# Optimization experiments

Hardware: AMD Instinct MI355X
Metric: run time of the kernel (lower is better)

## Reference

```python
import jax, jax.numpy as jnp
import numpy as np

B, S, D, H, FF = 2, 2048, 1024, 16, 4096
HD = D // H          # head dim = 64
ROT = HD // 2        # rotary dim = dim/(num_heads*2) = 32 (partial rotation)
EPS = 1e-5


def setup_inputs() -> dict:
    key = jax.random.key(0)
    ks = jax.random.split(key, 16)
    std = 0.02
    return {
        "x": jax.random.normal(ks[0], (B, S, D), jnp.float32),
        "mask": jnp.ones((B, 1, 1, S), jnp.int32),
        "wq": jax.random.normal(ks[1], (D, D), jnp.float32) * std,
        "bq": jnp.zeros((D,), jnp.float32),
        "wk": jax.random.normal(ks[2], (D, D), jnp.float32) * std,
        "bk": jnp.zeros((D,), jnp.float32),
        "wv": jax.random.normal(ks[3], (D, D), jnp.float32) * std,
        "bv": jnp.zeros((D,), jnp.float32),
        "wo": jax.random.normal(ks[4], (D, D), jnp.float32) * std,
        "bo": jnp.zeros((D,), jnp.float32),
        "ln1_w": jnp.ones((D,), jnp.float32),
        "ln1_b": jnp.zeros((D,), jnp.float32),
        "ln2_w": jnp.ones((D,), jnp.float32),
        "ln2_b": jnp.zeros((D,), jnp.float32),
        "w1": jax.random.normal(ks[5], (D, FF), jnp.float32) * std,
        "b1": jnp.zeros((FF,), jnp.float32),
        "w2": jax.random.normal(ks[6], (FF, D), jnp.float32) * std,
        "b2": jnp.zeros((D,), jnp.float32),
    }


def _layernorm(x, w, b):
    mu = jnp.mean(x, axis=-1, keepdims=True)
    var = jnp.mean(jnp.square(x - mu), axis=-1, keepdims=True)
    return (x - mu) * jax.lax.rsqrt(var + EPS) * w + b


def _rope(t):
    # t: [B, H, S, HD]; rotate first ROT features, interleaved (GPT-J) pairing
    inv_freq = 1.0 / (10000.0 ** (jnp.arange(0, ROT, 2, dtype=jnp.float32) / ROT))
    ang = jnp.arange(S, dtype=jnp.float32)[:, None] * inv_freq      # [S, ROT//2]
    ang = jnp.repeat(ang, 2, axis=-1)                               # [S, ROT]
    cos, sin = jnp.cos(ang), jnp.sin(ang)
    t_rot, t_pass = t[..., :ROT], t[..., ROT:]
    pr = t_rot.reshape(*t_rot.shape[:-1], ROT // 2, 2)
    rot = jnp.stack([-pr[..., 1], pr[..., 0]], axis=-1).reshape(t_rot.shape)
    return jnp.concatenate([t_rot * cos + rot * sin, t_pass], axis=-1)


def reference(x, mask, wq, bq, wk, bk, wv, bv, wo, bo,
              ln1_w, ln1_b, ln2_w, ln2_b, w1, b1, w2, b2):
    res = x
    h = _layernorm(x, ln1_w, ln1_b)
    q = (h @ wq + bq).reshape(B, S, H, HD).transpose(0, 2, 1, 3)
    k = (h @ wk + bk).reshape(B, S, H, HD).transpose(0, 2, 1, 3)
    v = (h @ wv + bv).reshape(B, S, H, HD).transpose(0, 2, 1, 3)
    q, k = _rope(q), _rope(k)
    score = jnp.einsum('bhqd,bhkd->bhqk', q, k) * (1.0 / np.sqrt(HD))
    score = jnp.where(mask == 0, jnp.float32(-1e9), score)
    attn = jax.nn.softmax(score, axis=-1)
    out = jnp.einsum('bhqk,bhkd->bhqd', attn, v)
    out = out.transpose(0, 2, 1, 3).reshape(B, S, D) @ wo + bo
    x = res + out
    res = x
    h = _layernorm(x, ln2_w, ln2_b)
    h = jax.nn.gelu(h @ w1 + b1, approximate=False) @ w2 + b2
    return res + h
```

## Files before the change

kernel.cpp:

```cpp
#include <hip/hip_runtime.h>
#include <cstdint>
#include <cstddef>


typedef __bf16 bf16;
typedef __bf16 bf16x2 __attribute__((ext_vector_type(2)));
typedef __bf16 bf16x4v __attribute__((ext_vector_type(4)));
typedef __bf16 bf16x8 __attribute__((ext_vector_type(8)));
typedef float  f32x4  __attribute__((ext_vector_type(4)));

#define NB 2
#define NS 2048
#define ND 1024
#define NH 16
#define NHD 64
#define NFF 4096
#define NM (NB*NS)
#define QKSCALE 0.18033688011112042f

typedef uint32_t __attribute__((address_space(1))) gu32_t;
typedef uint32_t __attribute__((address_space(3))) lu32_t;
__device__ __forceinline__ void async_copy16(void* lds, const void* g) {
  __builtin_amdgcn_global_load_lds((gu32_t*)g, (lu32_t*)lds, 16, 0, 0);
}

__device__ __forceinline__ float gelu_f(float x) {
  return 0.5f * x * (1.0f + erff(x * 0.70710678118654752f));
}

__global__ __launch_bounds__(256) void prep_kernel(
    const float* __restrict__ wq, const float* __restrict__ wk,
    const float* __restrict__ wv, const float* __restrict__ wo,
    const float* __restrict__ w1, const float* __restrict__ w2,
    bf16* __restrict__ wqt, bf16* __restrict__ wkt, bf16* __restrict__ wvt,
    bf16* __restrict__ wot, bf16* __restrict__ w1t, bf16* __restrict__ w2t,
    const float* __restrict__ bq, const float* __restrict__ bk,
    const float* __restrict__ bv, float* __restrict__ bcat,
    const int* __restrict__ mask, float* __restrict__ m01f,
    bf16* __restrict__ m01b, float2* __restrict__ rtab,
    const float* __restrict__ x, const float* __restrict__ ln1w,
    const float* __restrict__ ln1b, bf16* __restrict__ h1) {
  int flat = blockIdx.x;
  int t = threadIdx.x;
  if (flat < 12288) {
    __shared__ float tile[32][33];
    const float* W; bf16* Wt; long bx, by; int K, N;
    if (flat < 4096) {
      int which = flat >> 10, r = flat & 1023;
      const float* Ws[4] = {wq, wk, wv, wo};
      bf16* Wts[4] = {wqt, wkt, wvt, wot};
      W = Ws[which]; Wt = Wts[which]; bx = r & 31; by = r >> 5; K = ND; N = ND;
    } else if (flat < 8192) {
      int r = flat - 4096;
      W = w1; Wt = w1t; bx = r & 127; by = r >> 7; K = ND; N = NFF;
    } else {
      int r = flat - 8192;
      W = w2; Wt = w2t; bx = r & 31; by = r >> 5; K = NFF; N = ND;
    }
    int tx = t & 31, ty = t >> 5;
#pragma unroll
    for (int r = 0; r < 4; ++r)
      tile[ty + r*8][tx] = W[(by*32 + ty + r*8) * (long)N + bx*32 + tx];
    __syncthreads();
#pragma unroll
    for (int r = 0; r < 4; ++r)
      Wt[(bx*32 + ty + r*8) * (long)K + by*32 + tx] = (bf16)tile[tx][ty + r*8];
  } else if (flat < 12444) {
    int blk = flat - 12288;
    if (blk < 12) {
      int i = blk * 256 + t;
      bcat[i] = (i < ND) ? bq[i] : ((i < 2*ND) ? bk[i - ND] : bv[i - 2*ND]);
    } else if (blk < 28) {
      int i = (blk - 12) * 256 + t;
      float v = mask[i] ? 1.0f : 0.0f;
      m01f[i] = v;
      m01b[i] = (bf16)v;
    } else {
      int idx = (blk - 28) * 256 + t;
      int s = idx >> 4, i = idx & 15;
      float ang = (float)s * exp2f(-(float)i * (13.287712379549449f / 16.0f));
      float sn, cs;
      sincosf(ang, &sn, &cs);
      rtab[idx] = make_float2(cs, sn);
    }
  } else {
    long row = flat - 12444;
    float4 v = ((const float4*)(x + row*ND))[t];
    float s  = v.x + v.y + v.z + v.w;
    float sq = v.x*v.x + v.y*v.y + v.z*v.z + v.w*v.w;
#pragma unroll
    for (int m = 1; m <= 32; m <<= 1) { s += __shfl_xor(s, m); sq += __shfl_xor(sq, m); }
    __shared__ float ss[4], ssq[4];
    if ((t & 63) == 0) { ss[t>>6] = s; ssq[t>>6] = sq; }
    __syncthreads();
    s  = ss[0] + ss[1] + ss[2] + ss[3];
    sq = ssq[0] + ssq[1] + ssq[2] + ssq[3];
    float mu = s * (1.0f/ND);
    float rs = rsqrtf(sq * (1.0f/ND) - mu*mu + 1e-5f);
    float4 wv4 = ((const float4*)ln1w)[t];
    float4 bv4 = ((const float4*)ln1b)[t];
    bf16x4v o;
    o[0] = (bf16)((v.x-mu)*rs*wv4.x + bv4.x);
    o[1] = (bf16)((v.y-mu)*rs*wv4.y + bv4.y);
    o[2] = (bf16)((v.z-mu)*rs*wv4.z + bv4.z);
    o[3] = (bf16)((v.w-mu)*rs*wv4.w + bv4.w);
    *(bf16x4v*)(h1 + row*ND + t*4) = o;
  }
}

__global__ __launch_bounds__(256) void vtrans_kernel(
    const bf16* __restrict__ v, bf16* __restrict__ vt) {
  __shared__ bf16 t[64][66];
  int st = blockIdx.x, bh = blockIdx.y;
  int b = bh >> 4, h = bh & 15;
  int c = threadIdx.x & 63, rg = threadIdx.x >> 6;
  const bf16* src = v + ((long)b*NS + st*64)*ND + h*64;
#pragma unroll
  for (int i = 0; i < 16; ++i) {
    int r = rg*16 + i;
    t[r][c] = src[(long)r*ND + c];
  }
  __syncthreads();
  bf16* dst = vt + (long)bh*64*NS + st*64;
#pragma unroll
  for (int i = 0; i < 16; ++i) {
    int d = rg*16 + i;
    dst[(long)d*NS + c] = t[c][d];
  }
}

__global__ __launch_bounds__(256) void ln_kernel(
    const float* __restrict__ x, const float* __restrict__ w,
    const float* __restrict__ b, bf16* __restrict__ out) {
  long row = blockIdx.x;
  int t = threadIdx.x;
  float4 v = ((const float4*)(x + row*ND))[t];
  float s  = v.x + v.y + v.z + v.w;
  float sq = v.x*v.x + v.y*v.y + v.z*v.z + v.w*v.w;
#pragma unroll
  for (int m = 1; m <= 32; m <<= 1) { s += __shfl_xor(s, m); sq += __shfl_xor(sq, m); }
  __shared__ float ss[4], ssq[4];
  if ((t & 63) == 0) { ss[t>>6] = s; ssq[t>>6] = sq; }
  __syncthreads();
  s  = ss[0] + ss[1] + ss[2] + ss[3];
  sq = ssq[0] + ssq[1] + ssq[2] + ssq[3];
  float mu = s * (1.0f/ND);
  float rs = rsqrtf(sq * (1.0f/ND) - mu*mu + 1e-5f);
  float4 wv = ((const float4*)w)[t];
  float4 bv = ((const float4*)b)[t];
  bf16x4v o;
  o[0] = (bf16)((v.x-mu)*rs*wv.x + bv.x);
  o[1] = (bf16)((v.y-mu)*rs*wv.y + bv.y);
  o[2] = (bf16)((v.z-mu)*rs*wv.z + bv.z);
  o[3] = (bf16)((v.w-mu)*rs*wv.w + bv.w);
  *(bf16x4v*)(out + row*ND + t*4) = o;
}

__global__ __launch_bounds__(256) void ffn2red_kernel(
    const float* __restrict__ P, const float* __restrict__ y1,
    const float* __restrict__ b2, float* __restrict__ out) {
  const long n4 = (long)NM * ND / 4;
  const float4* p = (const float4*)P;
  const float4* y = (const float4*)y1;
  const float4* bb = (const float4*)b2;
  float4* o = (float4*)out;
  for (long i = (long)blockIdx.x*256 + threadIdx.x; i < n4;
       i += (long)gridDim.x*256) {
    float4 a0 = p[i], a1 = p[i + n4], a2 = p[i + 2*n4], a3 = p[i + 3*n4];
    float4 yv = y[i];
    float4 bv = bb[i & 255];
    float4 r;
    r.x = (a0.x + a1.x) + (a2.x + a3.x) + yv.x + bv.x;
    r.y = (a0.y + a1.y) + (a2.y + a3.y) + yv.y + bv.y;
    r.z = (a0.z + a1.z) + (a2.z + a3.z) + yv.z + bv.z;
    r.w = (a0.w + a1.w) + (a2.w + a3.w) + yv.w + bv.w;
    o[i] = r;
  }
}

template<int EPI>
__global__ __launch_bounds__(512, 2) void gemm256_kernel(
    const bf16* __restrict__ A, const bf16* __restrict__ Bt,
    const float* __restrict__ bias, void* __restrict__ Cout,
    const float2* __restrict__ rtab, const float* __restrict__ m01f,
    int M, int N, int K, int lda, int ldbt) {
  __shared__ __align__(16) bf16 Alds[2][256*32];
  __shared__ __align__(16) bf16 Blds[2][256*32];
  const int tid = threadIdx.x, lane = tid & 63, w = tid >> 6;
  const int fr = lane & 15, kg = lane >> 4;
  const int wr = w >> 2, wc = w & 3;
  const int swb = (kg ^ ((fr >> 1) & 3)) << 4;
  const int kz = (EPI == 2) ? blockIdx.z : 0;
  const long kofs = (long)kz * K;

  const int gx = gridDim.x;
  int lin = blockIdx.y * gx + blockIdx.x;
  int nwg = gx * gridDim.y;
  int swz = (lin & 7) * (nwg >> 3) + (lin >> 3);
  const long am0 = (long)(swz / gx) * 256;
  const long bn0 = (long)(swz % gx) * 256;

  const f32x4 fzero = {0.f, 0.f, 0.f, 0.f};
  f32x4 acc[8][4];
#pragma unroll
  for (int m = 0; m < 8; ++m)
#pragma unroll
    for (int n = 0; n < 4; ++n) acc[m][n] = fzero;

  auto stage = [&](int kt, int bufi) {
#pragma unroll
    for (int i = 0; i < 2; ++i) {
      int s = i*512 + tid;
      int r = s >> 2, c = (s & 3) ^ ((s >> 3) & 3);
      async_copy16((char*)&Alds[bufi][0] + i*8192 + w*1024,
                   &A[(am0 + r)*(long)lda + kofs + kt + c*8]);
      async_copy16((char*)&Blds[bufi][0] + i*8192 + w*1024,
                   &Bt[(bn0 + r)*(long)ldbt + kofs + kt + c*8]);
    }
  };

  const int nk = K >> 5;
  stage(0, 0);
  asm volatile("s_waitcnt vmcnt(0)" ::: "memory");
  __builtin_amdgcn_s_barrier();
  __builtin_amdgcn_sched_barrier(0);

  for (int t = 0; t < nk; ++t) {
    const int cur = t & 1;
    if (t + 1 < nk) stage((t + 1) * 32, cur ^ 1);
    const char* Ab = (const char*)&Alds[cur][0];
    const char* Bb = (const char*)&Blds[cur][0];
    bf16x8 af[4], bfv[4];
#pragma unroll
    for (int n = 0; n < 4; ++n) bfv[n] = *(const bf16x8*)(Bb + (wc*64 + n*16 + fr)*64 + swb);
#pragma unroll
    for (int m = 0; m < 4; ++m) af[m]  = *(const bf16x8*)(Ab + (wr*128 + m*16 + fr)*64 + swb);
    asm volatile("s_waitcnt lgkmcnt(0)" ::: "memory");
    __builtin_amdgcn_sched_barrier(0);
    __builtin_amdgcn_s_setprio(1);
#pragma unroll
    for (int m = 0; m < 4; ++m)
#pragma unroll
      for (int n = 0; n < 4; ++n)
        acc[m][n] = __builtin_amdgcn_mfma_f32_16x16x32_bf16(af[m], bfv[n], acc[m][n], 0, 0, 0);
    __builtin_amdgcn_s_setprio(0);
#pragma unroll
    for (int m = 0; m < 4; ++m) af[m] = *(const bf16x8*)(Ab + (wr*128 + (m+4)*16 + fr)*64 + swb);
    asm volatile("s_waitcnt lgkmcnt(0)" ::: "memory");
    __builtin_amdgcn_sched_barrier(0);
    __builtin_amdgcn_s_setprio(1);
#pragma unroll
    for (int m = 0; m < 4; ++m)
#pragma unroll
      for (int n = 0; n < 4; ++n)
        acc[m+4][n] = __builtin_amdgcn_mfma_f32_16x16x32_bf16(af[m], bfv[n], acc[m+4][n], 0, 0, 0);
    __builtin_amdgcn_s_setprio(0);
    asm volatile("s_waitcnt vmcnt(0)" ::: "memory");
    __builtin_amdgcn_s_barrier();
    __builtin_amdgcn_sched_barrier(0);
  }

  const int rbase = kg * 4;
  const int region = (int)(bn0 >> 10);
#pragma unroll
  for (int m = 0; m < 8; ++m) {
#pragma unroll
    for (int n = 0; n < 4; ++n) {
      long col = bn0 + wc*64 + n*16 + fr;
      float bia = (EPI == 2) ? 0.0f : bias[col];
#pragma unroll
      for (int j = 0; j < 4; ++j) {
        long row = am0 + wr*128 + m*16 + rbase + j;
        float val = acc[m][n][j] + bia;
        if (EPI == 1) {
          ((bf16*)Cout)[row * N + col] = (bf16)gelu_f(val);
        } else if (EPI == 2) {
          ((float*)Cout)[((long)kz * NM + row) * N + col] = val;
        } else {
          long cv = col & 1023;
          if (region <= 1) {
            float pval = __shfl_xor(val, 1);
            if (n < 2) {
              float2 cs = rtab[((row & (NS-1)) << 4) | ((n*16 + fr) >> 1)];
              val = (fr & 1) ? val*cs.x + pval*cs.y : val*cs.x - pval*cs.y;
            }
            if (region == 0) val *= QKSCALE;
          } else {
            val *= m01f[row];
          }
          ((bf16*)Cout)[(long)region * (NM*(long)ND) + row * ND + cv] = (bf16)val;
        }
      }
    }
  }
}

__global__ __launch_bounds__(512, 1) void gemm128x8_kernel(
    const bf16* __restrict__ A, const bf16* __restrict__ Bt,
    const float* __restrict__ bias, const float* __restrict__ res,
    float* __restrict__ Cout, int M, int N, int K) {
  __shared__ __align__(16) bf16 Alds[4][128*64];
  __shared__ __align__(16) bf16 Blds[4][128*64];
  const int tid = threadIdx.x, lane = tid & 63, w = tid >> 6;
  const int fr = lane & 15, kg = lane >> 4;
  const int wr = w >> 1, wc = w & 1;

  const int gx = gridDim.x;
  int lin = blockIdx.y * gx + blockIdx.x;
  int nwg = gx * gridDim.y;
  int swz = (lin & 7) * (nwg >> 3) + (lin >> 3);
  const long am0 = (long)(swz / gx) * 128;
  const long bn0 = (long)(swz % gx) * 128;

  const f32x4 fzero = {0.f, 0.f, 0.f, 0.f};
  f32x4 acc[2][4];
#pragma unroll
  for (int m = 0; m < 2; ++m)
#pragma unroll
    for (int n = 0; n < 4; ++n) acc[m][n] = fzero;

  auto stage = [&](int kt, int bufi) {
#pragma unroll
    for (int i = 0; i < 2; ++i) {
      int s = i*512 + tid;
      int r = s >> 3, c = (s & 7) ^ (r & 7);
      async_copy16((char*)&Alds[bufi][0] + i*8192 + w*1024,
                   &A[(am0 + r)*K + kt + c*8]);
      async_copy16((char*)&Blds[bufi][0] + i*8192 + w*1024,
                   &Bt[(bn0 + r)*K + kt + c*8]);
    }
  };

  const int nk = K >> 6;
  stage(0, 0);
  stage(64, 1);
  asm volatile("s_waitcnt vmcnt(4)" ::: "memory");
  __builtin_amdgcn_s_barrier();
  __builtin_amdgcn_sched_barrier(0);

  for (int t = 0; t < nk; ++t) {
    const int cur = t & 3;
    if (t + 2 < nk) stage((t + 2) * 64, (t + 2) & 3);
    const char* Ab = (const char*)&Alds[cur][0];
    const char* Bb = (const char*)&Blds[cur][0];
    bf16x8 af[2][2], bfv[2][4];
#pragma unroll
    for (int kk = 0; kk < 2; ++kk) {
#pragma unroll
      for (int m = 0; m < 2; ++m) {
        int r = wr*32 + m*16 + fr;
        af[kk][m] = *(const bf16x8*)(Ab + r*128 + (((kk*4 + kg) ^ (r & 7)) << 4));
      }
#pragma unroll
      for (int n = 0; n < 4; ++n) {
        int r = wc*64 + n*16 + fr;
        bfv[kk][n] = *(const bf16x8*)(Bb + r*128 + (((kk*4 + kg) ^ (r & 7)) << 4));
      }
    }
    asm volatile("s_waitcnt lgkmcnt(0)" ::: "memory");
    __builtin_amdgcn_sched_barrier(0);
    __builtin_amdgcn_s_setprio(1);
#pragma unroll
    for (int kk = 0; kk < 2; ++kk)
#pragma unroll
      for (int m = 0; m < 2; ++m)
#pragma unroll
        for (int n = 0; n < 4; ++n)
          acc[m][n] = __builtin_amdgcn_mfma_f32_16x16x32_bf16(af[kk][m], bfv[kk][n], acc[m][n], 0, 0, 0);
    __builtin_amdgcn_s_setprio(0);
    if (t + 2 < nk) { asm volatile("s_waitcnt vmcnt(4)" ::: "memory"); }
    else            { asm volatile("s_waitcnt vmcnt(0)" ::: "memory"); }
    __builtin_amdgcn_s_barrier();
    __builtin_amdgcn_sched_barrier(0);
  }

  const int rbase = kg * 4;
#pragma unroll
  for (int m = 0; m < 2; ++m) {
#pragma unroll
    for (int n = 0; n < 4; ++n) {
      long col = bn0 + wc*64 + n*16 + fr;
      float bia = bias[col];
#pragma unroll
      for (int j = 0; j < 4; ++j) {
        long row = am0 + wr*32 + m*16 + rbase + j;
        Cout[row * N + col] = acc[m][n][j] + bia + res[row * N + col];
      }
    }
  }
}

__global__ __launch_bounds__(512) void attn_kernel(
    const bf16* __restrict__ q, const bf16* __restrict__ k,
    const bf16* __restrict__ vt, const bf16* __restrict__ m01b,
    bf16* __restrict__ out) {
  int lin = blockIdx.y * 16 + blockIdx.x;
  int swz = (lin & 7) * 64 + (lin >> 3);
  const int qt = swz & 15;
  const int bh = swz >> 4;
  const int b = bh >> 4, h = bh & 15;
  const int tid = threadIdx.x, lane = tid & 63, w = tid >> 6;
  const int fr = lane & 15, kg = lane >> 4;
  const int k8 = kg * 8;
  const int frl = fr & 3, frh = fr >> 2;

  __shared__ __align__(16) bf16 Klds[3][64*64];
  __shared__ __align__(16) bf16 Vlds[3][64*64];
  __shared__ __align__(16) bf16 Mlds[NS];

  const long qrow = (long)qt*128 + w*16 + fr;
  const bf16* qbase = q + ((long)b*NS + qrow)*ND + h*NHD;
  bf16x8 qf[2];
  qf[0] = *(const bf16x8*)(qbase + k8);
  qf[1] = *(const bf16x8*)(qbase + 32 + k8);

  const bf16* kbase = k + (long)b*NS*ND + h*NHD;
  const bf16* vtb = vt + (long)bh*64*NS;
  const bf16* mbase = m01b + (long)b*NS;

  if (w < 4) async_copy16((char*)Mlds + w*1024, mbase + tid*8);

  const int srow = tid >> 3, sc = tid & 7;
  const int csK = (sc ^ (srow & 7) ^ (((srow >> 3) & 1) << 2));
  const int csV = (sc ^ (srow & 7));
  auto stageK = [&](int kt, int bufi) {
    async_copy16((char*)&Klds[bufi][0] + w*1024,
                 kbase + ((long)kt*64 + srow)*ND + csK*8);
  };
  auto stageV = [&](int kt, int bufi) {
    async_copy16((char*)&Vlds[bufi][0] + w*1024,
                 vtb + (long)srow*NS + kt*64 + csV*8);
  };

  const f32x4 fzero = {0.f, 0.f, 0.f, 0.f};
  f32x4 oacc[4], oaccL = fzero;
#pragma unroll
  for (int n = 0; n < 4; ++n) oacc[n] = fzero;

  stageK(0, 0); stageV(0, 0);
  stageK(1, 1); stageV(1, 1);
  asm volatile("s_waitcnt vmcnt(2)" ::: "memory");
  __builtin_amdgcn_s_barrier();
  __builtin_amdgcn_sched_barrier(0);

  const int NT = NS / 64;
  int bcur = 0, bpre = 1;
  for (int kt = 0; kt < NT; ++kt) {
    if (kt + 2 < NT) {
      bpre = (bpre == 2) ? 0 : bpre + 1;
      stageK(kt + 2, bpre);
      stageV(kt + 2, bpre);
    }
    const char* Kb = (const char*)&Klds[bcur][0];
    const char* Vb = (const char*)&Vlds[bcur][0];

    bf16x8 vbm0 = *(const bf16x8*)&Mlds[kt*64 + k8];
    bf16x8 vbm1 = *(const bf16x8*)&Mlds[kt*64 + 32 + k8];

    f32x4 sacc[4];
#pragma unroll
    for (int n = 0; n < 4; ++n) sacc[n] = fzero;
#pragma unroll
    for (int n = 0; n < 4; ++n) {
      int r = (frh << 3) + ((n & 1) << 2) + frl + ((n >> 1) << 5);
      int swzr = (r & 7) ^ (((r >> 3) & 1) << 2);
#pragma unroll
      for (int kk = 0; kk < 2; ++kk) {
        bf16x8 kf = *(const bf16x8*)(Kb + r*128 + ((((kk << 2) | kg) ^ swzr) << 4));
        sacc[n] = __builtin_amdgcn_mfma_f32_16x16x32_bf16(kf, qf[kk], sacc[n], 0, 0, 0);
      }
    }

    float p[4][4];
#pragma unroll
    for (int n = 0; n < 4; ++n) {
      p[n][0] = exp2f(sacc[n][0]);
      p[n][1] = exp2f(sacc[n][1]);
      p[n][2] = exp2f(sacc[n][2]);
      p[n][3] = exp2f(sacc[n][3]);
    }

    bf16x8 paf[2];
#pragma unroll
    for (int n = 0; n < 4; ++n) {
#pragma unroll
      for (int j = 0; j < 4; ++j)
        paf[n >> 1][((n & 1) << 2) + j] = (bf16)p[n][j];
    }

    oaccL = __builtin_amdgcn_mfma_f32_16x16x32_bf16(paf[0], vbm0, oaccL, 0, 0, 0);
    oaccL = __builtin_amdgcn_mfma_f32_16x16x32_bf16(paf[1], vbm1, oaccL, 0, 0, 0);

#pragma unroll
    for (int kk = 0; kk < 2; ++kk) {
#pragma unroll
      for (int n2 = 0; n2 < 4; ++n2) {
        int r = n2*16 + fr;
        bf16x8 vb8 = *(const bf16x8*)(Vb + r*128 + ((((kk << 2) | kg) ^ (r & 7)) << 4));
        oacc[n2] = __builtin_amdgcn_mfma_f32_16x16x32_bf16(paf[kk], vb8, oacc[n2], 0, 0, 0);
      }
    }

    if (kt + 2 < NT)      { asm volatile("s_waitcnt vmcnt(2)" ::: "memory"); }
    else if (kt + 1 < NT) { asm volatile("s_waitcnt vmcnt(0)" ::: "memory"); }
    __builtin_amdgcn_s_barrier();
    __builtin_amdgcn_sched_barrier(0);
    bcur = (bcur == 2) ? 0 : bcur + 1;
  }

#pragma unroll
  for (int j = 0; j < 4; ++j) {
    float inv = 1.0f / oaccL[j];
    long orow = (long)qt*128 + w*16 + kg*4 + j;
    bf16* ob = out + ((long)b*NS + orow)*ND + h*NHD;
#pragma unroll
    for (int n2 = 0; n2 < 4; ++n2) ob[n2*16 + fr] = (bf16)(oacc[n2][j] * inv);
  }
}

extern "C" void kernel_launch(void* const* d_in, const int* in_sizes, int n_in,
                              void* d_out, int out_size, void* d_ws, size_t ws_size,
                              hipStream_t stream) {
  const float* x    = (const float*)d_in[0];
  const int*   mask = (const int*)d_in[1];
  const float* wq   = (const float*)d_in[2];
  const float* bq   = (const float*)d_in[3];
  const float* wk   = (const float*)d_in[4];
  const float* bk   = (const float*)d_in[5];
  const float* wv   = (const float*)d_in[6];
  const float* bv   = (const float*)d_in[7];
  const float* wo   = (const float*)d_in[8];
  const float* bo   = (const float*)d_in[9];
  const float* ln1w = (const float*)d_in[10];
  const float* ln1b = (const float*)d_in[11];
  const float* ln2w = (const float*)d_in[12];
  const float* ln2b = (const float*)d_in[13];
  const float* w1   = (const float*)d_in[14];
  const float* b1   = (const float*)d_in[15];
  const float* w2   = (const float*)d_in[16];
  const float* b2   = (const float*)d_in[17];
  float* out = (float*)d_out;

  char* ws = (char*)d_ws;
  const size_t MB = 1024ull * 1024ull;
  bf16* wqt = (bf16*)(ws + 0*MB);
  bf16* wkt = (bf16*)(ws + 2*MB);
  bf16* wvt = (bf16*)(ws + 4*MB);
  bf16* wot = (bf16*)(ws + 6*MB);
  bf16* w1t = (bf16*)(ws + 8*MB);
  bf16* w2t = (bf16*)(ws + 16*MB);
  bf16* h1   = (bf16*)(ws + 24*MB);
  bf16* qb   = (bf16*)(ws + 32*MB);
  bf16* kb   = (bf16*)(ws + 40*MB);
  bf16* vb   = (bf16*)(ws + 48*MB);
  bf16* vtb  = h1;
  bf16* attnb = (bf16*)(ws + 72*MB);
  bf16* f1   = (bf16*)(ws + 24*MB);
  float* y1  = (float*)(ws + 56*MB);
  bf16* h2   = (bf16*)(ws + 72*MB);
  float* bcat = (float*)(ws + 80*MB);
  float* m01f = (float*)(ws + 80*MB + 16*1024);
  bf16*  m01b = (bf16*) (ws + 80*MB + 32*1024);
  float2* rtab = (float2*)(ws + 80*MB + 48*1024);
  float* pK   = (float*)(ws + 84*MB);
  const bool use_splitk = (ws_size >= 148ull*MB);
  (void)in_sizes; (void)n_in; (void)out_size;

  prep_kernel<<<16540, 256, 0, stream>>>(wq, wk, wv, wo, w1, w2,
                                         wqt, wkt, wvt, wot, w1t, w2t,
                                         bq, bk, bv, bcat, mask, m01f, m01b,
                                         rtab, x, ln1w, ln1b, h1);

  gemm256_kernel<3><<<dim3(12, 16), 512, 0, stream>>>(h1, wqt, bcat, qb,
                                                      rtab, m01f, NM, 3*ND, ND,
                                                      ND, ND);
  vtrans_kernel<<<dim3(32, 32), 256, 0, stream>>>(vb, vtb);

  attn_kernel<<<dim3(16, 32), 512, 0, stream>>>(qb, kb, vtb, m01b, attnb);

  gemm128x8_kernel<<<dim3(8, 32), 512, 0, stream>>>(attnb, wot, bo, x, y1,
                                                    NM, ND, ND);
  ln_kernel<<<NM, 256, 0, stream>>>(y1, ln2w, ln2b, h2);
  gemm256_kernel<1><<<dim3(16, 16), 512, 0, stream>>>(h2, w1t, b1, f1,
                                                      nullptr, nullptr,
                                                      NM, NFF, ND, ND, ND);
  if (use_splitk) {
    gemm256_kernel<2><<<dim3(4, 16, 4), 512, 0, stream>>>(f1, w2t, nullptr, pK,
                                                          nullptr, nullptr,
                                                          NM, ND, ND, NFF, NFF);
    ffn2red_kernel<<<2048, 256, 0, stream>>>(pK, y1, b2, out);
  } else {
    gemm128x8_kernel<<<dim3(8, 32), 512, 0, stream>>>(f1, w2t, b2, y1, out,
                                                      NM, ND, NFF);
  }
}
```

Measured before the change: 292.0 us.

## Deepen GEMM K-tile to 64 and prefetch two stages ahead

```diff
diff --git a/kernel.cpp b/kernel.cpp
--- a/kernel.cpp
+++ b/kernel.cpp
@@ -184,12 +184,11 @@
     const float* __restrict__ bias, void* __restrict__ Cout,
     const float2* __restrict__ rtab, const float* __restrict__ m01f,
     int M, int N, int K, int lda, int ldbt) {
-  __shared__ __align__(16) bf16 Alds[2][256*32];
-  __shared__ __align__(16) bf16 Blds[2][256*32];
+  __shared__ __align__(16) bf16 Alds[2][256*64];
+  __shared__ __align__(16) bf16 Blds[2][256*64];
   const int tid = threadIdx.x, lane = tid & 63, w = tid >> 6;
   const int fr = lane & 15, kg = lane >> 4;
   const int wr = w >> 2, wc = w & 3;
-  const int swb = (kg ^ ((fr >> 1) & 3)) << 4;
   const int kz = (EPI == 2) ? blockIdx.z : 0;
   const long kofs = (long)kz * K;
 
@@ -209,32 +208,42 @@
 
   auto stage = [&](int kt, int bufi) {
 #pragma unroll
-    for (int i = 0; i < 2; ++i) {
+    for (int i = 0; i < 4; ++i) {
       int s = i*512 + tid;
-      int r = s >> 2, c = (s & 3) ^ ((s >> 3) & 3);
+      int r = s >> 3, c = (s & 7) ^ (r & 7);
       async_copy16((char*)&Alds[bufi][0] + i*8192 + w*1024,
                    &A[(am0 + r)*(long)lda + kofs + kt + c*8]);
+    }
+#pragma unroll
+    for (int i = 0; i < 4; ++i) {
+      int s = i*512 + tid;
+      int r = s >> 3, c = (s & 7) ^ (r & 7);
       async_copy16((char*)&Blds[bufi][0] + i*8192 + w*1024,
                    &Bt[(bn0 + r)*(long)ldbt + kofs + kt + c*8]);
     }
   };
 
-  const int nk = K >> 5;
+  const int nk = K >> 6;
   stage(0, 0);
-  asm volatile("s_waitcnt vmcnt(0)" ::: "memory");
+  stage(64, 1);
+  asm volatile("s_waitcnt vmcnt(8)" ::: "memory");
   __builtin_amdgcn_s_barrier();
   __builtin_amdgcn_sched_barrier(0);
 
   for (int t = 0; t < nk; ++t) {
-    const int cur = t & 1;
-    if (t + 1 < nk) stage((t + 1) * 32, cur ^ 1);
-    const char* Ab = (const char*)&Alds[cur][0];
-    const char* Bb = (const char*)&Blds[cur][0];
-    bf16x8 af[4], bfv[4];
-#pragma unroll
-    for (int n = 0; n < 4; ++n) bfv[n] = *(const bf16x8*)(Bb + (wc*64 + n*16 + fr)*64 + swb);
-#pragma unroll
-    for (int m = 0; m < 4; ++m) af[m]  = *(const bf16x8*)(Ab + (wr*128 + m*16 + fr)*64 + swb);
+    const char* Ab = (const char*)&Alds[t & 1][0];
+    const char* Bb = (const char*)&Blds[t & 1][0];
+    bf16x8 bfv0[4], bfv1[4], af[4];
+#pragma unroll
+    for (int n = 0; n < 4; ++n) {
+      int r = wc*64 + n*16 + fr;
+      bfv0[n] = *(const bf16x8*)(Bb + r*128 + ((kg ^ (r & 7)) << 4));
+    }
+#pragma unroll
+    for (int m = 0; m < 4; ++m) {
+      int r = wr*128 + m*16 + fr;
+      af[m] = *(const bf16x8*)(Ab + r*128 + ((kg ^ (r & 7)) << 4));
+    }
     asm volatile("s_waitcnt lgkmcnt(0)" ::: "memory");
     __builtin_amdgcn_sched_barrier(0);
     __builtin_amdgcn_s_setprio(1);
@@ -242,10 +251,18 @@
     for (int m = 0; m < 4; ++m)
 #pragma unroll
       for (int n = 0; n < 4; ++n)
-        acc[m][n] = __builtin_amdgcn_mfma_f32_16x16x32_bf16(af[m], bfv[n], acc[m][n], 0, 0, 0);
+        acc[m][n] = __builtin_amdgcn_mfma_f32_16x16x32_bf16(af[m], bfv0[n], acc[m][n], 0, 0, 0);
     __builtin_amdgcn_s_setprio(0);
 #pragma unroll
-    for (int m = 0; m < 4; ++m) af[m] = *(const bf16x8*)(Ab + (wr*128 + (m+4)*16 + fr)*64 + swb);
+    for (int n = 0; n < 4; ++n) {
+      int r = wc*64 + n*16 + fr;
+      bfv1[n] = *(const bf16x8*)(Bb + r*128 + (((4 + kg) ^ (r & 7)) << 4));
+    }
+#pragma unroll
+    for (int m = 0; m < 4; ++m) {
+      int r = wr*128 + m*16 + fr;
+      af[m] = *(const bf16x8*)(Ab + r*128 + (((4 + kg) ^ (r & 7)) << 4));
+    }
     asm volatile("s_waitcnt lgkmcnt(0)" ::: "memory");
     __builtin_amdgcn_sched_barrier(0);
     __builtin_amdgcn_s_setprio(1);
@@ -253,9 +270,46 @@
     for (int m = 0; m < 4; ++m)
 #pragma unroll
       for (int n = 0; n < 4; ++n)
-        acc[m+4][n] = __builtin_amdgcn_mfma_f32_16x16x32_bf16(af[m], bfv[n], acc[m+4][n], 0, 0, 0);
+        acc[m][n] = __builtin_amdgcn_mfma_f32_16x16x32_bf16(af[m], bfv1[n], acc[m][n], 0, 0, 0);
     __builtin_amdgcn_s_setprio(0);
-    asm volatile("s_waitcnt vmcnt(0)" ::: "memory");
+#pragma unroll
+    for (int m = 0; m < 4; ++m) {
+      int r = wr*128 + (m+4)*16 + fr;
+      af[m] = *(const bf16x8*)(Ab + r*128 + ((kg ^ (r & 7)) << 4));
+    }
+    asm volatile("s_waitcnt lgkmcnt(0)" ::: "memory");
+    __builtin_amdgcn_sched_barrier(0);
+    __builtin_amdgcn_s_setprio(1);
+#pragma unroll
+    for (int m = 0; m < 4; ++m)
+#pragma unroll
+      for (int n = 0; n < 4; ++n)
+        acc[m+4][n] = __builtin_amdgcn_mfma_f32_16x16x32_bf16(af[m], bfv0[n], acc[m+4][n], 0, 0, 0);
+    __builtin_amdgcn_s_setprio(0);
+#pragma unroll
+    for (int m = 0; m < 4; ++m) {
+      int r = wr*128 + (m+4)*16 + fr;
+      af[m] = *(const bf16x8*)(Ab + r*128 + (((4 + kg) ^ (r & 7)) << 4));
+    }
+    asm volatile("s_waitcnt lgkmcnt(0)" ::: "memory");
+    __builtin_amdgcn_sched_barrier(0);
+    __builtin_amdgcn_s_setprio(1);
+#pragma unroll
+    for (int m = 0; m < 4; ++m)
+#pragma unroll
+      for (int n = 0; n < 4; ++n)
+        acc[m+4][n] = __builtin_amdgcn_mfma_f32_16x16x32_bf16(af[m], bfv1[n], acc[m+4][n], 0, 0, 0);
+    __builtin_amdgcn_s_setprio(0);
+
+    if (t + 1 == nk) break;
+    __builtin_amdgcn_s_barrier();
+    __builtin_amdgcn_sched_barrier(0);
+    if (t + 2 < nk) {
+      stage((t + 2) * 64, t & 1);
+      asm volatile("s_waitcnt vmcnt(8)" ::: "memory");
+    } else {
+      asm volatile("s_waitcnt vmcnt(0)" ::: "memory");
+    }
     __builtin_amdgcn_s_barrier();
     __builtin_amdgcn_sched_barrier(0);
   }
```

Result: faster. 274.2 us (-6.1%).

## Deepen GEMM LDS pipeline to four buffers and store split-K partials in bf16

Applied to the files above, without the earlier changes.

```diff
diff --git a/kernel.cpp b/kernel.cpp
--- a/kernel.cpp
+++ b/kernel.cpp
@@ -157,24 +157,31 @@
 }
 
 __global__ __launch_bounds__(256) void ffn2red_kernel(
-    const float* __restrict__ P, const float* __restrict__ y1,
+    const bf16* __restrict__ P, const float* __restrict__ y1,
     const float* __restrict__ b2, float* __restrict__ out) {
-  const long n4 = (long)NM * ND / 4;
-  const float4* p = (const float4*)P;
-  const float4* y = (const float4*)y1;
-  const float4* bb = (const float4*)b2;
-  float4* o = (float4*)out;
-  for (long i = (long)blockIdx.x*256 + threadIdx.x; i < n4;
+  const long n8 = (long)NM * ND / 8;
+  for (long i = (long)blockIdx.x*256 + threadIdx.x; i < n8;
        i += (long)gridDim.x*256) {
-    float4 a0 = p[i], a1 = p[i + n4], a2 = p[i + 2*n4], a3 = p[i + 3*n4];
-    float4 yv = y[i];
-    float4 bv = bb[i & 255];
-    float4 r;
-    r.x = (a0.x + a1.x) + (a2.x + a3.x) + yv.x + bv.x;
-    r.y = (a0.y + a1.y) + (a2.y + a3.y) + yv.y + bv.y;
-    r.z = (a0.z + a1.z) + (a2.z + a3.z) + yv.z + bv.z;
-    r.w = (a0.w + a1.w) + (a2.w + a3.w) + yv.w + bv.w;
-    o[i] = r;
+    bf16x8 p0 = ((const bf16x8*)P)[i];
+    bf16x8 p1 = ((const bf16x8*)P)[i + n8];
+    bf16x8 p2 = ((const bf16x8*)P)[i + 2*n8];
+    bf16x8 p3 = ((const bf16x8*)P)[i + 3*n8];
+    float4 ya = ((const float4*)y1)[2*i];
+    float4 yb = ((const float4*)y1)[2*i + 1];
+    int cb = (int)((i * 8) & 1023);
+    float4 ba = *(const float4*)&b2[cb];
+    float4 bb = *(const float4*)&b2[cb + 4];
+    float4 ra, rb;
+    ra.x = ((float)p0[0]+(float)p1[0])+((float)p2[0]+(float)p3[0]) + ya.x + ba.x;
+    ra.y = ((float)p0[1]+(float)p1[1])+((float)p2[1]+(float)p3[1]) + ya.y + ba.y;
+    ra.z = ((float)p0[2]+(float)p1[2])+((float)p2[2]+(float)p3[2]) + ya.z + ba.z;
+    ra.w = ((float)p0[3]+(float)p1[3])+((float)p2[3]+(float)p3[3]) + ya.w + ba.w;
+    rb.x = ((float)p0[4]+(float)p1[4])+((float)p2[4]+(float)p3[4]) + yb.x + bb.x;
+    rb.y = ((float)p0[5]+(float)p1[5])+((float)p2[5]+(float)p3[5]) + yb.y + bb.y;
+    rb.z = ((float)p0[6]+(float)p1[6])+((float)p2[6]+(float)p3[6]) + yb.z + bb.z;
+    rb.w = ((float)p0[7]+(float)p1[7])+((float)p2[7]+(float)p3[7]) + yb.w + bb.w;
+    ((float4*)out)[2*i]     = ra;
+    ((float4*)out)[2*i + 1] = rb;
   }
 }
 
@@ -184,12 +191,11 @@
     const float* __restrict__ bias, void* __restrict__ Cout,
     const float2* __restrict__ rtab, const float* __restrict__ m01f,
     int M, int N, int K, int lda, int ldbt) {
-  __shared__ __align__(16) bf16 Alds[2][256*32];
-  __shared__ __align__(16) bf16 Blds[2][256*32];
+  __shared__ __align__(16) bf16 Alds[4][256*32];
+  __shared__ __align__(16) bf16 Blds[4][256*32];
   const int tid = threadIdx.x, lane = tid & 63, w = tid >> 6;
   const int fr = lane & 15, kg = lane >> 4;
   const int wr = w >> 2, wc = w & 3;
-  const int swb = (kg ^ ((fr >> 1) & 3)) << 4;
   const int kz = (EPI == 2) ? blockIdx.z : 0;
   const long kofs = (long)kz * K;
 
@@ -211,7 +217,7 @@
 #pragma unroll
     for (int i = 0; i < 2; ++i) {
       int s = i*512 + tid;
-      int r = s >> 2, c = (s & 3) ^ ((s >> 3) & 3);
+      int r = s >> 2, c = (s & 3) ^ ((r >> 1) & 3);
       async_copy16((char*)&Alds[bufi][0] + i*8192 + w*1024,
                    &A[(am0 + r)*(long)lda + kofs + kt + c*8]);
       async_copy16((char*)&Blds[bufi][0] + i*8192 + w*1024,
@@ -221,20 +227,27 @@
 
   const int nk = K >> 5;
   stage(0, 0);
-  asm volatile("s_waitcnt vmcnt(0)" ::: "memory");
+  stage(32, 1);
+  asm volatile("s_waitcnt vmcnt(4)" ::: "memory");
   __builtin_amdgcn_s_barrier();
   __builtin_amdgcn_sched_barrier(0);
 
-  for (int t = 0; t < nk; ++t) {
-    const int cur = t & 1;
-    if (t + 1 < nk) stage((t + 1) * 32, cur ^ 1);
-    const char* Ab = (const char*)&Alds[cur][0];
-    const char* Bb = (const char*)&Blds[cur][0];
-    bf16x8 af[4], bfv[4];
-#pragma unroll
-    for (int n = 0; n < 4; ++n) bfv[n] = *(const bf16x8*)(Bb + (wc*64 + n*16 + fr)*64 + swb);
-#pragma unroll
-    for (int m = 0; m < 4; ++m) af[m]  = *(const bf16x8*)(Ab + (wr*128 + m*16 + fr)*64 + swb);
+  for (int s = 0; s < nk; ++s) {
+    const char* Ab = (const char*)&Alds[s & 3][0];
+    const char* Bb = (const char*)&Blds[s & 3][0];
+    bf16x8 bfv[4], af[4];
+#pragma unroll
+    for (int n = 0; n < 4; ++n) {
+      int r = wc*64 + n*16 + fr;
+      bfv[n] = *(const bf16x8*)(Bb + r*64 + ((kg ^ ((r >> 1) & 3)) << 4));
+    }
+#pragma unroll
+    for (int m = 0; m < 4; ++m) {
+      int r = wr*128 + m*16 + fr;
+      af[m] = *(const bf16x8*)(Ab + r*64 + ((kg ^ ((r >> 1) & 3)) << 4));
+    }
+    if (s + 2 < nk) stage((s + 2) * 32, (s + 2) & 3);
+    __builtin_amdgcn_s_barrier();
     asm volatile("s_waitcnt lgkmcnt(0)" ::: "memory");
     __builtin_amdgcn_sched_barrier(0);
     __builtin_amdgcn_s_setprio(1);
@@ -244,8 +257,13 @@
       for (int n = 0; n < 4; ++n)
         acc[m][n] = __builtin_amdgcn_mfma_f32_16x16x32_bf16(af[m], bfv[n], acc[m][n], 0, 0, 0);
     __builtin_amdgcn_s_setprio(0);
-#pragma unroll
-    for (int m = 0; m < 4; ++m) af[m] = *(const bf16x8*)(Ab + (wr*128 + (m+4)*16 + fr)*64 + swb);
+    __builtin_amdgcn_s_barrier();
+#pragma unroll
+    for (int m = 0; m < 4; ++m) {
+      int r = wr*128 + (m+4)*16 + fr;
+      af[m] = *(const bf16x8*)(Ab + r*64 + ((kg ^ ((r >> 1) & 3)) << 4));
+    }
+    __builtin_amdgcn_s_barrier();
     asm volatile("s_waitcnt lgkmcnt(0)" ::: "memory");
     __builtin_amdgcn_sched_barrier(0);
     __builtin_amdgcn_s_setprio(1);
@@ -255,7 +273,10 @@
       for (int n = 0; n < 4; ++n)
         acc[m+4][n] = __builtin_amdgcn_mfma_f32_16x16x32_bf16(af[m], bfv[n], acc[m+4][n], 0, 0, 0);
     __builtin_amdgcn_s_setprio(0);
-    asm volatile("s_waitcnt vmcnt(0)" ::: "memory");
+
+    if (s + 1 == nk) break;
+    if (s + 2 < nk) { asm volatile("s_waitcnt vmcnt(4)" ::: "memory"); }
+    else            { asm volatile("s_waitcnt vmcnt(0)" ::: "memory"); }
     __builtin_amdgcn_s_barrier();
     __builtin_amdgcn_sched_barrier(0);
   }
@@ -275,7 +296,7 @@
         if (EPI == 1) {
           ((bf16*)Cout)[row * N + col] = (bf16)gelu_f(val);
         } else if (EPI == 2) {
-          ((float*)Cout)[((long)kz * NM + row) * N + col] = val;
+          ((bf16*)Cout)[((long)kz * NM + row) * N + col] = (bf16)val;
         } else {
           long cv = col & 1023;
           if (region <= 1) {
@@ -562,8 +583,8 @@
   float* m01f = (float*)(ws + 80*MB + 16*1024);
   bf16*  m01b = (bf16*) (ws + 80*MB + 32*1024);
   float2* rtab = (float2*)(ws + 80*MB + 48*1024);
-  float* pK   = (float*)(ws + 84*MB);
-  const bool use_splitk = (ws_size >= 148ull*MB);
+  bf16* pK   = (bf16*)(ws + 84*MB);
+  const bool use_splitk = (ws_size >= 116ull*MB);
   (void)in_sizes; (void)n_in; (void)out_size;
 
   prep_kernel<<<16540, 256, 0, stream>>>(wq, wk, wv, wo, w1, w2,
```

Result: faster. 277.2 us (-5.1%).
